# Performance work log

Hardware: AMD Instinct MI355X
Metric: run time of the kernel (lower is better)

Reference implementation:

```python
import jax, jax.numpy as jnp
import numpy as np

B, D, F, K = 16384, 768, 8192, 32

def setup_inputs() -> dict:
    key = jax.random.key(0)
    k0, k1, k2 = jax.random.split(key, 3)
    x = jax.random.normal(k0, (B, D), dtype=jnp.float32)
    # encoder weight ~ orthogonal-ish scale; exact init scheme doesn't affect the math being tested
    W_enc = jax.random.normal(k1, (F, D), dtype=jnp.float32) / np.sqrt(D)
    b_enc = jnp.zeros((F,), dtype=jnp.float32)
    W_dec = jax.random.normal(k2, (D, F), dtype=jnp.float32)
    # torch init normalizes decoder.weight rows (dim=1)
    W_dec = W_dec / jnp.linalg.norm(W_dec, axis=1, keepdims=True)
    dec_bias = jnp.zeros((D,), dtype=jnp.float32)
    return {"x": x, "W_enc": W_enc, "b_enc": b_enc, "W_dec": W_dec, "dec_bias": dec_bias, "k": K}


def reference(x, W_enc, b_enc, W_dec, dec_bias, k):
    # encode: center, linear, relu
    x_centered = x - dec_bias                              # [B, D]
    acts = jax.nn.relu(jnp.einsum('bd,fd->bf', x_centered, W_enc) + b_enc)  # [B, F]
    # topk + scatter into dense sparse code
    vals, idx = jax.lax.top_k(acts, k)                     # [B, k]
    rows = jnp.arange(acts.shape[0])[:, None]              # [B, 1]
    sparse_code = jnp.zeros_like(acts).at[rows, idx].set(vals)  # [B, F]
    # decode: dense GEMM over mostly-zero code + bias
    reconstruction = jnp.einsum('bf,df->bd', sparse_code, W_dec) + dec_bias  # [B, D]
    return reconstruction, sparse_code
```

## Files before the change

kernel.cpp:

```cpp
#include <hip/hip_runtime.h>

#define NB 16384
#define ND 768
#define NF 8192
#define CMAX 512
#define AMAX 128
#define MARG 0.07f

typedef __attribute__((ext_vector_type(8))) short bf16x8;
typedef __attribute__((ext_vector_type(4))) float f32x4;
typedef __attribute__((ext_vector_type(4))) unsigned int u32x4;
typedef __attribute__((ext_vector_type(2))) float f32x2;

__device__ inline unsigned short f2bf(float f) {
  unsigned u = __float_as_uint(f);
  unsigned r = (u + 0x7FFFu + ((u >> 16) & 1u)) >> 16;
  return (unsigned short)r;
}
__device__ inline float bfbits2f(unsigned u16) { return __uint_as_float(u16 << 16); }

__global__ __launch_bounds__(256) void cvt_bf16_k(const float* __restrict__ in,
                                                  unsigned short* __restrict__ out) {
  size_t t = (size_t)blockIdx.x * 256 + threadIdx.x;
  const float4* i4 = (const float4*)in;
  float4 a = i4[t * 2], b = i4[t * 2 + 1];
  ushort4 lo = make_ushort4(f2bf(a.x), f2bf(a.y), f2bf(a.z), f2bf(a.w));
  ushort4 hi = make_ushort4(f2bf(b.x), f2bf(b.y), f2bf(b.z), f2bf(b.w));
  ((ushort4*)out)[t * 2] = lo;
  ((ushort4*)out)[t * 2 + 1] = hi;
}

__global__ __launch_bounds__(256) void beta_k(const float* __restrict__ W_enc,
                                              const float* __restrict__ b_enc,
                                              const float* __restrict__ dec_bias,
                                              float* __restrict__ beta) {
  int f = blockIdx.x * 4 + (threadIdx.x >> 6);
  int lane = threadIdx.x & 63;
  const float* wr = W_enc + (size_t)f * ND;
  float s = 0.f;
  for (int d = lane; d < ND; d += 64) s += dec_bias[d] * wr[d];
  for (int off = 32; off; off >>= 1) s += __shfl_down(s, off);
  if (lane == 0) beta[f] = b_enc[f] - s;
}

__global__ __launch_bounds__(256) void transpose_bf_k(const float* __restrict__ in,
                                                      unsigned short* __restrict__ out) {
  __shared__ float tile[32][33];
  int lx = threadIdx.x & 31;
  int ty = threadIdx.x >> 5;
  int x = blockIdx.x * 32 + lx;
  for (int j = ty; j < 32; j += 8) {
    int y = blockIdx.y * 32 + j;
    tile[j][lx] = in[(size_t)y * NF + x];
  }
  __syncthreads();
  int xo = blockIdx.y * 32 + lx;
  for (int j = ty; j < 32; j += 8) {
    int yo = blockIdx.x * 32 + j;
    out[(size_t)yo * ND + xo] = f2bf(tile[lx][j]);
  }
}

__global__ __launch_bounds__(256) void enc_gemm_bf16(
    const unsigned short* __restrict__ Xb, const unsigned short* __restrict__ Wb,
    const float* __restrict__ beta, unsigned short* __restrict__ acts,
    unsigned short* __restrict__ tmax) {
  __shared__ __align__(1024) unsigned short SL[2][128 * 64];
  unsigned short* As = SL[0];
  unsigned short* Bs = SL[1];
  const int tid = threadIdx.x;
  const int wave = tid >> 6, lane = tid & 63;
  const int wm = wave >> 1, wn = wave & 1;

  const int orig = blockIdx.y * gridDim.x + blockIdx.x;
  const int xcd = orig & 7;
  const int local = orig >> 3;
  const int tcol = local >> 4;
  const int trow = (xcd << 4) + (local & 15);
  const int brow = trow << 7;
  const int bcol = tcol << 7;

  f32x4 acc[4][4] = {};

  const int srow = tid >> 3;
  const int scol = (((tid & 7) ^ ((tid >> 3) & 7)) << 3);
  const unsigned short* gA = Xb + (size_t)(brow + srow) * ND + scol;
  const unsigned short* gB = Wb + (size_t)(bcol + srow) * ND + scol;

  for (int kt = 0; kt < ND; kt += 64) {
#pragma unroll
    for (int i = 0; i < 4; ++i) {
      __builtin_amdgcn_global_load_lds(
          (const __attribute__((address_space(1))) void*)(gA + (size_t)(i * 32) * ND + kt),
          (__attribute__((address_space(3))) void*)(As + (i * 32 + wave * 8) * 64), 16, 0, 0);
      __builtin_amdgcn_global_load_lds(
          (const __attribute__((address_space(1))) void*)(gB + (size_t)(i * 32) * ND + kt),
          (__attribute__((address_space(3))) void*)(Bs + (i * 32 + wave * 8) * 64), 16, 0, 0);
    }
    __syncthreads();
#pragma unroll
    for (int kk = 0; kk < 64; kk += 32) {
      const int chunk = (kk + ((lane >> 4) << 3)) >> 3;
      const int rA = (wm << 6) + (lane & 15);
      const int rB = (wn << 6) + (lane & 15);
      const int sw = chunk ^ (lane & 7);
      bf16x8 a[4], bvv[4];
#pragma unroll
      for (int m = 0; m < 4; ++m)
        a[m] = *(const bf16x8*)&As[(rA + (m << 4)) * 64 + (sw << 3)];
#pragma unroll
      for (int n = 0; n < 4; ++n)
        bvv[n] = *(const bf16x8*)&Bs[(rB + (n << 4)) * 64 + (sw << 3)];
#pragma unroll
      for (int m = 0; m < 4; ++m)
#pragma unroll
        for (int n = 0; n < 4; ++n)
          acc[m][n] = __builtin_amdgcn_mfma_f32_16x16x32_bf16(a[m], bvv[n], acc[m][n], 0, 0, 0);
    }
    __syncthreads();
  }

  unsigned short* S = (unsigned short*)SL;
#pragma unroll
  for (int n = 0; n < 4; ++n) {
    float bet = beta[bcol + (wn << 6) + (n << 4) + (lane & 15)];
#pragma unroll
    for (int m = 0; m < 4; ++m) {
#pragma unroll
      for (int r = 0; r < 4; ++r) {
        int row_l = (wm << 6) + (m << 4) + ((lane >> 4) << 2) + r;
        int col_l = (wn << 6) + (n << 4) + (lane & 15);
        float v = fmaxf(acc[m][n][r] + bet, 0.f);
        int slot = (col_l >> 3) ^ (row_l & 7);
        S[row_l * 128 + (slot << 3) + (col_l & 7)] = f2bf(v);
      }
    }
  }
  __syncthreads();
#pragma unroll
  for (int i = 0; i < 8; ++i) {
    int row_l = (tid >> 4) + (i << 4);
    int slot = tid & 15;
    u32x4 d = *(const u32x4*)&S[row_l * 128 + (slot << 3)];
    unsigned mx = 0;
#pragma unroll
    for (int q = 0; q < 4; ++q) {
      unsigned lo = d[q] & 0xFFFFu, hi = d[q] >> 16;
      if (lo > mx) mx = lo;
      if (hi > mx) mx = hi;
    }
#pragma unroll
    for (int off = 1; off < 16; off <<= 1) {
      unsigned o = __shfl_xor(mx, off);
      if (o > mx) mx = o;
    }
    int chunk = slot ^ (row_l & 7);
    __builtin_nontemporal_store(
        d, (u32x4*)&acts[(size_t)(brow + row_l) * NF + bcol + (chunk << 3)]);
    if (slot == 0) tmax[(size_t)(brow + row_l) * 64 + tcol] = (unsigned short)mx;
  }
}

__global__ __launch_bounds__(256) void tkth_k(const unsigned short* __restrict__ tmax,
                                              const int* __restrict__ kptr,
                                              float* __restrict__ Lthr) {
  const int wave = threadIdx.x >> 6, lane = threadIdx.x & 63;
  const int b = blockIdx.x * 4 + wave;
  int k = *kptr; k = k < 1 ? 1 : (k > 64 ? 64 : k);
  unsigned key = tmax[(size_t)b * 64 + lane];
  unsigned T = 0;
  for (int bit = 14; bit >= 0; --bit) {
    unsigned probe = T | (1u << bit);
    int c = __popcll(__ballot(key >= probe));
    if (c >= k) T = probe;
  }
  if (lane == 0) Lthr[b] = bfbits2f(T) - MARG;
}

__global__ __launch_bounds__(256, 6) void ksel_k(
    const unsigned short* __restrict__ acts, const unsigned short* __restrict__ tmax,
    const float* __restrict__ Lthr, const float* __restrict__ x,
    const float* __restrict__ W_enc, const float* __restrict__ beta,
    const unsigned short* __restrict__ WdecBf, const float* __restrict__ dec_bias,
    const int* __restrict__ kptr,
    float* __restrict__ out_rec, float* __restrict__ g_vals, int* __restrict__ g_idxs) {
  const int tid = threadIdx.x, wave = tid >> 6, lane = tid & 63;
  const int b = blockIdx.x * 4 + wave;
  int k = *kptr; k = k < 1 ? 1 : (k > 64 ? 64 : k);
  const unsigned kk = (unsigned)k;

  __shared__ int stile_s[4][64];
  __shared__ unsigned clist_s[4][CMAX];
  __shared__ unsigned long long aval_s[4][AMAX];
  __shared__ float selv_s[4][64];
  __shared__ int seli_s[4][64];
  __shared__ int ctrC_s[4], ctrW_s[4], ctrA_s[4];

  int* stile = stile_s[wave];
  unsigned* clist = clist_s[wave];
  unsigned long long* aval = aval_s[wave];
  float* selv = selv_s[wave];
  int* seli = seli_s[wave];

  if (lane == 0) { ctrC_s[wave] = 0; ctrW_s[wave] = 0; ctrA_s[wave] = 0; }
  const float Lf = Lthr[b];

  {
    unsigned short tm = tmax[(size_t)b * 64 + lane];
    bool sel = bfbits2f(tm) >= Lf;
    unsigned long long mask = __ballot(sel);
    int pos = __popcll(mask & ((1ull << lane) - 1ull));
    if (sel) stile[pos] = lane;
  }
  __syncthreads();
  const int nsel = __popcll(__ballot(bfbits2f(tmax[(size_t)b * 64 + lane]) >= Lf));

  const u32x4* row16 = (const u32x4*)(acts + (size_t)b * NF);
  for (int t = 0; t < nsel; t += 4) {
    int tt = t + (lane >> 4);
    if (tt < nsel) {
      int tile = stile[tt];
      u32x4 v = __builtin_nontemporal_load(&row16[tile * 16 + (lane & 15)]);
      int base = tile * 128 + (lane & 15) * 8;
#pragma unroll
      for (int q = 0; q < 4; ++q) {
#pragma unroll
        for (int h = 0; h < 2; ++h) {
          unsigned u = h ? (v[q] >> 16) : (v[q] & 0xFFFFu);
          if (bfbits2f(u) >= Lf) {
            int p = atomicAdd(&ctrC_s[wave], 1);
            if (p < CMAX) clist[p] = (u << 16) | (unsigned)(base + q * 2 + h);
          }
        }
      }
    }
  }
  __syncthreads();
  int n = ctrC_s[wave]; if (n > CMAX) n = CMAX;

  unsigned ks[8];
#pragma unroll
  for (int ii = 0; ii < 8; ++ii) {
    int j = lane + (ii << 6);
    ks[ii] = (j < n) ? (clist[j] >> 16) : 0u;
  }
  unsigned T = 0;
  for (int bit = 14; bit >= 0; --bit) {
    unsigned probe = T | (1u << bit);
    int c = 0;
#pragma unroll
    for (int ii = 0; ii < 8; ++ii) c += (ks[ii] >= probe);
#pragma unroll
    for (int off = 32; off; off >>= 1) c += __shfl_xor(c, off);
    if (c >= (int)kk) T = probe;
  }
  const float tauf = bfbits2f(T);
  const float thrW = tauf + MARG;
  const float thrA = tauf - MARG;

  for (int j = lane; j < n; j += 64) {
    unsigned e = clist[j];
    float v = bfbits2f(e >> 16);
    int idx = (int)(e & 0xFFFFu);
    if (v > thrW) {
      int p = atomicAdd(&ctrW_s[wave], 1);
      if (p < 63) { selv[p] = v; seli[p] = idx; }
    } else if (v >= thrA) {
      int p = atomicAdd(&ctrA_s[wave], 1);
      if (p < AMAX) aval[p] = (unsigned long long)(unsigned)idx;
    }
  }
  __syncthreads();
  int c = ctrW_s[wave]; if (c > 63) c = 63; if (c > k - 1) c = k - 1;
  int na = ctrA_s[wave]; if (na > AMAX) na = AMAX;

  float xr[12];
#pragma unroll
  for (int cc = 0; cc < 12; ++cc)
    xr[cc] = __builtin_nontemporal_load(&x[(size_t)b * ND + lane + 64 * cc]);
  for (int j = 0; j < na; j += 2) {
    int f0 = (int)(unsigned)aval[j];
    int f1 = (j + 1 < na) ? (int)(unsigned)aval[j + 1] : f0;
    const float* w0 = W_enc + (size_t)f0 * ND;
    const float* w1 = W_enc + (size_t)f1 * ND;
    float s0 = 0.f, s1 = 0.f;
#pragma unroll
    for (int cc = 0; cc < 12; ++cc) {
      s0 = fmaf(xr[cc], w0[lane + 64 * cc], s0);
      s1 = fmaf(xr[cc], w1[lane + 64 * cc], s1);
    }
#pragma unroll
    for (int off = 32; off; off >>= 1) {
      s0 += __shfl_xor(s0, off);
      s1 += __shfl_xor(s1, off);
    }
    if (lane == 0) {
      float v0 = fmaxf(s0 + beta[f0], 0.f);
      aval[j] = (((unsigned long long)__float_as_uint(v0)) << 13) | (unsigned)(8191 - f0);
      if (j + 1 < na) {
        float v1 = fmaxf(s1 + beta[f1], 0.f);
        aval[j + 1] = (((unsigned long long)__float_as_uint(v1)) << 13) | (unsigned)(8191 - f1);
      }
    }
  }
  __syncthreads();

  {
    unsigned long long p0 = (lane < na) ? aval[lane] : 0ull;
    unsigned long long p1 = (lane + 64 < na) ? aval[lane + 64] : 0ull;
    int rounds = k - c; if (rounds < 0) rounds = 0;
    for (int r = 0; r < rounds; ++r) {
      unsigned long long m = p0 > p1 ? p0 : p1;
#pragma unroll
      for (int off = 32; off; off >>= 1) {
        unsigned long long o = __shfl_xor(m, off);
        if (o > m) m = o;
      }
      if (lane == 0) {
        if (m) { selv[c + r] = __uint_as_float((unsigned)(m >> 13)); seli[c + r] = 8191 - (int)(m & 0x1FFFull); }
        else   { selv[c + r] = 0.f; seli[c + r] = 0; }
      }
      if (p0 == m) p0 = 0;
      if (p1 == m) p1 = 0;
    }
  }
  __syncthreads();

  if (lane < k) {
    g_vals[(size_t)b * 64 + lane] = selv[lane];
    g_idxs[(size_t)b * 64 + lane] = seli[lane];
  }

  float acc[12];
#pragma unroll
  for (int cc = 0; cc < 6; ++cc) {
    float2 db = *(const float2*)&dec_bias[cc * 128 + lane * 2];
    acc[2 * cc] = db.x; acc[2 * cc + 1] = db.y;
  }
#define RECON_TERM(r)                                                          \
  {                                                                            \
    int f = seli[r]; float v = selv[r];                                        \
    const unsigned short* wd = WdecBf + (size_t)f * ND;                        \
    _Pragma("unroll")                                                          \
    for (int cc = 0; cc < 6; ++cc) {                                           \
      unsigned pr = *(const unsigned*)&wd[cc * 128 + lane * 2];                \
      acc[2 * cc] = fmaf(v, bfbits2f(pr & 0xFFFFu), acc[2 * cc]);              \
      acc[2 * cc + 1] = fmaf(v, bfbits2f(pr >> 16), acc[2 * cc + 1]);          \
    }                                                                          \
  }
  if (k == 32) {
#pragma unroll
    for (int r = 0; r < 32; ++r) RECON_TERM(r)
  } else {
    for (int r = 0; r < k; ++r) RECON_TERM(r)
  }
#pragma unroll
  for (int cc = 0; cc < 6; ++cc) {
    f32x2 st = {acc[2 * cc], acc[2 * cc + 1]};
    __builtin_nontemporal_store(st, (f32x2*)&out_rec[(size_t)b * ND + cc * 128 + lane * 2]);
  }
}

__global__ __launch_bounds__(256) void d2_sparse_k(
    const float* __restrict__ g_vals, const int* __restrict__ g_idxs,
    const int* __restrict__ kptr, float* __restrict__ out_sc) {
  const int b = blockIdx.x, tid = threadIdx.x;
  int k = *kptr; k = k < 1 ? 1 : (k > 64 ? 64 : k);
  __shared__ float row[NF];
  __shared__ float sv[64];
  __shared__ int si[64];
  if (tid < k) { sv[tid] = g_vals[(size_t)b * 64 + tid]; si[tid] = g_idxs[(size_t)b * 64 + tid]; }
  float4* r4 = (float4*)row;
#pragma unroll
  for (int i = 0; i < 8; ++i) r4[tid + 256 * i] = make_float4(0.f, 0.f, 0.f, 0.f);
  __syncthreads();
  if (tid < k) row[si[tid]] = sv[tid];
  __syncthreads();
  f32x4* o4 = (f32x4*)(out_sc + (size_t)b * NF);
  const f32x4* r4v = (const f32x4*)row;
#pragma unroll
  for (int i = 0; i < 8; ++i)
    __builtin_nontemporal_store(r4v[tid + 256 * i], &o4[tid + 256 * i]);
}

extern "C" void kernel_launch(void* const* d_in, const int* in_sizes, int n_in,
                              void* d_out, int out_size, void* d_ws, size_t ws_size,
                              hipStream_t stream) {
  const float* x        = (const float*)d_in[0];
  const float* W_enc    = (const float*)d_in[1];
  const float* b_enc    = (const float*)d_in[2];
  const float* W_dec    = (const float*)d_in[3];
  const float* dec_bias = (const float*)d_in[4];
  const int*   kptr     = (const int*)d_in[5];

  float* out_rec = (float*)d_out;
  float* out_sc  = (float*)d_out + (size_t)NB * ND;

  char* scb = (char*)out_sc;
  unsigned short* acts = (unsigned short*)scb;
  unsigned short* Xbf  = (unsigned short*)(scb + 268435456);
  unsigned short* Wbf  = (unsigned short*)(scb + 293601280);

  char* ws = (char*)d_ws;
  unsigned short* WdecBf = (unsigned short*)ws;
  float* beta   = (float*)(ws + 12582912);
  float* g_vals = (float*)(ws + 12615680);
  int*   g_idxs = (int*)(ws + 16809984);
  unsigned short* tmax = (unsigned short*)(ws + 21004288);
  float* Lthr  = (float*)(ws + 23101440);

  cvt_bf16_k<<<(NB * ND) / 2048, 256, 0, stream>>>(x, Xbf);
  cvt_bf16_k<<<(NF * ND) / 2048, 256, 0, stream>>>(W_enc, Wbf);
  beta_k<<<NF / 4, 256, 0, stream>>>(W_enc, b_enc, dec_bias, beta);
  transpose_bf_k<<<dim3(NF / 32, ND / 32), 256, 0, stream>>>(W_dec, WdecBf);
  enc_gemm_bf16<<<dim3(NF / 128, NB / 128), 256, 0, stream>>>(Xbf, Wbf, beta, acts, tmax);
  tkth_k<<<NB / 4, 256, 0, stream>>>(tmax, kptr, Lthr);
  ksel_k<<<NB / 4, 256, 0, stream>>>(acts, tmax, Lthr, x, W_enc, beta, WdecBf, dec_bias,
                                     kptr, out_rec, g_vals, g_idxs);
  d2_sparse_k<<<NB, 256, 0, stream>>>(g_vals, g_idxs, kptr, out_sc);
}
```

Baseline: 601.9 us.

## Collect above-threshold candidates in GEMM epilogue, skip per-row acts rescan

The encoder GEMM epilogue now appends every activation at or above a fixed threshold (2.0) to a per-row global candidate list using global atomics. The top-k selection kernel reads this list directly instead of recomputing a tile threshold and rescanning the bf16 activation rows, and the separate threshold kernel is removed. A fallback path runs the old scan for any block where the list overflowed, held too few entries, or the resulting tau is too close to the fixed threshold. The cost is many global atomics in the GEMM epilogue, an extra zeroing kernel, and a threshold constant tuned to the input distribution.

```diff
diff --git a/kernel.cpp b/kernel.cpp
--- a/kernel.cpp
+++ b/kernel.cpp
@@ -6,6 +6,8 @@
 #define CMAX 512
 #define AMAX 128
 #define MARG 0.07f
+#define THETA0 2.0f
+#define THETA0_BITS 0x4000u
 
 typedef __attribute__((ext_vector_type(8))) short bf16x8;
 typedef __attribute__((ext_vector_type(4))) float f32x4;
@@ -18,6 +20,10 @@
   return (unsigned short)r;
 }
 __device__ inline float bfbits2f(unsigned u16) { return __uint_as_float(u16 << 16); }
+
+__global__ __launch_bounds__(256) void zerocnt_k(unsigned* __restrict__ gcnt) {
+  gcnt[blockIdx.x * 256 + threadIdx.x] = 0u;
+}
 
 __global__ __launch_bounds__(256) void cvt_bf16_k(const float* __restrict__ in,
                                                   unsigned short* __restrict__ out) {
@@ -64,7 +70,8 @@
 __global__ __launch_bounds__(256) void enc_gemm_bf16(
     const unsigned short* __restrict__ Xb, const unsigned short* __restrict__ Wb,
     const float* __restrict__ beta, unsigned short* __restrict__ acts,
-    unsigned short* __restrict__ tmax) {
+    unsigned short* __restrict__ tmax,
+    unsigned* __restrict__ gcnt, unsigned* __restrict__ glist) {
   __shared__ __align__(1024) unsigned short SL[2][128 * 64];
   unsigned short* As = SL[0];
   unsigned short* Bs = SL[1];
@@ -131,8 +138,15 @@
         int row_l = (wm << 6) + (m << 4) + ((lane >> 4) << 2) + r;
         int col_l = (wn << 6) + (n << 4) + (lane & 15);
         float v = fmaxf(acc[m][n][r] + bet, 0.f);
+        unsigned short ub = f2bf(v);
         int slot = (col_l >> 3) ^ (row_l & 7);
-        S[row_l * 128 + (slot << 3) + (col_l & 7)] = f2bf(v);
+        S[row_l * 128 + (slot << 3) + (col_l & 7)] = ub;
+        if (ub >= (unsigned short)THETA0_BITS) {
+          unsigned p = atomicAdd(&gcnt[brow + row_l], 1u);
+          if (p < CMAX)
+            glist[(size_t)(brow + row_l) * CMAX + p] =
+                ((unsigned)ub << 16) | (unsigned)(bcol + col_l);
+        }
       }
     }
   }
@@ -161,28 +175,12 @@
   }
 }
 
-__global__ __launch_bounds__(256) void tkth_k(const unsigned short* __restrict__ tmax,
-                                              const int* __restrict__ kptr,
-                                              float* __restrict__ Lthr) {
-  const int wave = threadIdx.x >> 6, lane = threadIdx.x & 63;
-  const int b = blockIdx.x * 4 + wave;
-  int k = *kptr; k = k < 1 ? 1 : (k > 64 ? 64 : k);
-  unsigned key = tmax[(size_t)b * 64 + lane];
-  unsigned T = 0;
-  for (int bit = 14; bit >= 0; --bit) {
-    unsigned probe = T | (1u << bit);
-    int c = __popcll(__ballot(key >= probe));
-    if (c >= k) T = probe;
-  }
-  if (lane == 0) Lthr[b] = bfbits2f(T) - MARG;
-}
-
 __global__ __launch_bounds__(256, 6) void ksel_k(
     const unsigned short* __restrict__ acts, const unsigned short* __restrict__ tmax,
-    const float* __restrict__ Lthr, const float* __restrict__ x,
-    const float* __restrict__ W_enc, const float* __restrict__ beta,
-    const unsigned short* __restrict__ WdecBf, const float* __restrict__ dec_bias,
-    const int* __restrict__ kptr,
+    const unsigned* __restrict__ gcnt, const unsigned* __restrict__ glist,
+    const float* __restrict__ x, const float* __restrict__ W_enc,
+    const float* __restrict__ beta, const unsigned short* __restrict__ WdecBf,
+    const float* __restrict__ dec_bias, const int* __restrict__ kptr,
     float* __restrict__ out_rec, float* __restrict__ g_vals, int* __restrict__ g_idxs) {
   const int tid = threadIdx.x, wave = tid >> 6, lane = tid & 63;
   const int b = blockIdx.x * 4 + wave;
@@ -195,6 +193,7 @@
   __shared__ float selv_s[4][64];
   __shared__ int seli_s[4][64];
   __shared__ int ctrC_s[4], ctrW_s[4], ctrA_s[4];
+  __shared__ int blkFb;
 
   int* stile = stile_s[wave];
   unsigned* clist = clist_s[wave];
@@ -202,41 +201,13 @@
   float* selv = selv_s[wave];
   int* seli = seli_s[wave];
 
+  if (tid == 0) blkFb = 0;
   if (lane == 0) { ctrC_s[wave] = 0; ctrW_s[wave] = 0; ctrA_s[wave] = 0; }
-  const float Lf = Lthr[b];
-
-  {
-    unsigned short tm = tmax[(size_t)b * 64 + lane];
-    bool sel = bfbits2f(tm) >= Lf;
-    unsigned long long mask = __ballot(sel);
-    int pos = __popcll(mask & ((1ull << lane) - 1ull));
-    if (sel) stile[pos] = lane;
-  }
-  __syncthreads();
-  const int nsel = __popcll(__ballot(bfbits2f(tmax[(size_t)b * 64 + lane]) >= Lf));
-
-  const u32x4* row16 = (const u32x4*)(acts + (size_t)b * NF);
-  for (int t = 0; t < nsel; t += 4) {
-    int tt = t + (lane >> 4);
-    if (tt < nsel) {
-      int tile = stile[tt];
-      u32x4 v = __builtin_nontemporal_load(&row16[tile * 16 + (lane & 15)]);
-      int base = tile * 128 + (lane & 15) * 8;
-#pragma unroll
-      for (int q = 0; q < 4; ++q) {
-#pragma unroll
-        for (int h = 0; h < 2; ++h) {
-          unsigned u = h ? (v[q] >> 16) : (v[q] & 0xFFFFu);
-          if (bfbits2f(u) >= Lf) {
-            int p = atomicAdd(&ctrC_s[wave], 1);
-            if (p < CMAX) clist[p] = (u << 16) | (unsigned)(base + q * 2 + h);
-          }
-        }
-      }
-    }
-  }
-  __syncthreads();
-  int n = ctrC_s[wave]; if (n > CMAX) n = CMAX;
+
+  const int raw = (int)gcnt[b];
+  int n = raw < CMAX ? raw : CMAX;
+  for (int j = lane; j < n; j += 64) clist[j] = glist[(size_t)b * CMAX + j];
+  __syncthreads();
 
   unsigned ks[8];
 #pragma unroll
@@ -254,7 +225,70 @@
     for (int off = 32; off; off >>= 1) c += __shfl_xor(c, off);
     if (c >= (int)kk) T = probe;
   }
-  const float tauf = bfbits2f(T);
+  float tauf = bfbits2f(T);
+
+  bool valid = (raw <= CMAX) && (n >= k) && (tauf >= THETA0 + MARG);
+  if (lane == 0 && !valid) atomicOr(&blkFb, 1);
+  __syncthreads();
+
+  if (blkFb) {
+    unsigned tm = tmax[(size_t)b * 64 + lane];
+    unsigned T2 = 0;
+    for (int bit = 14; bit >= 0; --bit) {
+      unsigned probe = T2 | (1u << bit);
+      int c = __popcll(__ballot(tm >= probe));
+      if (c >= k) T2 = probe;
+    }
+    const float Lf = bfbits2f(T2) - MARG;
+    if (lane == 0) ctrC_s[wave] = 0;
+    {
+      bool sel = bfbits2f(tm) >= Lf;
+      unsigned long long mask = __ballot(sel);
+      int pos = __popcll(mask & ((1ull << lane) - 1ull));
+      if (sel) stile[pos] = lane;
+    }
+    __syncthreads();
+    const int nsel = __popcll(__ballot(bfbits2f(tm) >= Lf));
+    const u32x4* row16 = (const u32x4*)(acts + (size_t)b * NF);
+    for (int t = 0; t < nsel; t += 4) {
+      int tt = t + (lane >> 4);
+      if (tt < nsel) {
+        int tile = stile[tt];
+        u32x4 v = __builtin_nontemporal_load(&row16[tile * 16 + (lane & 15)]);
+        int base = tile * 128 + (lane & 15) * 8;
+#pragma unroll
+        for (int q = 0; q < 4; ++q) {
+#pragma unroll
+          for (int h = 0; h < 2; ++h) {
+            unsigned u = h ? (v[q] >> 16) : (v[q] & 0xFFFFu);
+            if (bfbits2f(u) >= Lf) {
+              int p = atomicAdd(&ctrC_s[wave], 1);
+              if (p < CMAX) clist[p] = (u << 16) | (unsigned)(base + q * 2 + h);
+            }
+          }
+        }
+      }
+    }
+    __syncthreads();
+    n = ctrC_s[wave]; if (n > CMAX) n = CMAX;
+#pragma unroll
+    for (int ii = 0; ii < 8; ++ii) {
+      int j = lane + (ii << 6);
+      ks[ii] = (j < n) ? (clist[j] >> 16) : 0u;
+    }
+    T = 0;
+    for (int bit = 14; bit >= 0; --bit) {
+      unsigned probe = T | (1u << bit);
+      int c = 0;
+#pragma unroll
+      for (int ii = 0; ii < 8; ++ii) c += (ks[ii] >= probe);
+#pragma unroll
+      for (int off = 32; off; off >>= 1) c += __shfl_xor(c, off);
+      if (c >= (int)kk) T = probe;
+    }
+    tauf = bfbits2f(T);
+  }
+
   const float thrW = tauf + MARG;
   const float thrA = tauf - MARG;
 
@@ -397,9 +431,11 @@
   float* out_sc  = (float*)d_out + (size_t)NB * ND;
 
   char* scb = (char*)out_sc;
-  unsigned short* acts = (unsigned short*)scb;
-  unsigned short* Xbf  = (unsigned short*)(scb + 268435456);
-  unsigned short* Wbf  = (unsigned short*)(scb + 293601280);
+  unsigned short* acts  = (unsigned short*)scb;
+  unsigned short* Xbf   = (unsigned short*)(scb + 268435456);
+  unsigned short* Wbf   = (unsigned short*)(scb + 293601280);
+  unsigned*       glist = (unsigned*)(scb + 306184192);
+  unsigned*       gcnt  = (unsigned*)(scb + 339738624);
 
   char* ws = (char*)d_ws;
   unsigned short* WdecBf = (unsigned short*)ws;
@@ -407,15 +443,15 @@
   float* g_vals = (float*)(ws + 12615680);
   int*   g_idxs = (int*)(ws + 16809984);
   unsigned short* tmax = (unsigned short*)(ws + 21004288);
-  float* Lthr  = (float*)(ws + 23101440);
-
+
+  zerocnt_k<<<64, 256, 0, stream>>>(gcnt);
   cvt_bf16_k<<<(NB * ND) / 2048, 256, 0, stream>>>(x, Xbf);
   cvt_bf16_k<<<(NF * ND) / 2048, 256, 0, stream>>>(W_enc, Wbf);
   beta_k<<<NF / 4, 256, 0, stream>>>(W_enc, b_enc, dec_bias, beta);
   transpose_bf_k<<<dim3(NF / 32, ND / 32), 256, 0, stream>>>(W_dec, WdecBf);
-  enc_gemm_bf16<<<dim3(NF / 128, NB / 128), 256, 0, stream>>>(Xbf, Wbf, beta, acts, tmax);
-  tkth_k<<<NB / 4, 256, 0, stream>>>(tmax, kptr, Lthr);
-  ksel_k<<<NB / 4, 256, 0, stream>>>(acts, tmax, Lthr, x, W_enc, beta, WdecBf, dec_bias,
-                                     kptr, out_rec, g_vals, g_idxs);
+  enc_gemm_bf16<<<dim3(NF / 128, NB / 128), 256, 0, stream>>>(Xbf, Wbf, beta, acts,
+                                                              tmax, gcnt, glist);
+  ksel_k<<<NB / 4, 256, 0, stream>>>(acts, tmax, gcnt, glist, x, W_enc, beta, WdecBf,
+                                     dec_bias, kptr, out_rec, g_vals, g_idxs);
   d2_sparse_k<<<NB, 256, 0, stream>>>(g_vals, g_idxs, kptr, out_sc);
 }
```

Measured after the change: 940.8 us. +56.3%, slower.

## Emit fixed-threshold candidate lists from encoder GEMM instead of full bf16 activations

Applied to the files above, without the earlier changes.

The encoder GEMM no longer writes the full bf16 activation matrix and per-tile maxima. In its epilogue it keeps only activations above a fixed threshold of 2.0, appending up to 16 per row-tile into a compact candidate list. The threshold kernel is removed and the selection kernel reads these compact lists directly. The GEMM main loop also gains double-buffered LDS staging. When a row's candidates are insufficient or overflow, a slow block-wide fallback recomputes the full row in fp32. This relies on the fixed threshold suiting the data distribution and adds a costly path for rows where it does not.

```diff
diff --git a/kernel.cpp b/kernel.cpp
--- a/kernel.cpp
+++ b/kernel.cpp
@@ -4,8 +4,12 @@
 #define ND 768
 #define NF 8192
 #define CMAX 512
+#define SEGW 16
+#define GSEG 1024
 #define AMAX 128
 #define MARG 0.07f
+#define THETA0 2.0f
+#define THETA0_BITS 0x4000u
 
 typedef __attribute__((ext_vector_type(8))) short bf16x8;
 typedef __attribute__((ext_vector_type(4))) float f32x4;
@@ -63,11 +67,11 @@
 
 __global__ __launch_bounds__(256) void enc_gemm_bf16(
     const unsigned short* __restrict__ Xb, const unsigned short* __restrict__ Wb,
-    const float* __restrict__ beta, unsigned short* __restrict__ acts,
-    unsigned short* __restrict__ tmax) {
-  __shared__ __align__(1024) unsigned short SL[2][128 * 64];
-  unsigned short* As = SL[0];
-  unsigned short* Bs = SL[1];
+    const float* __restrict__ beta, unsigned* __restrict__ glist) {
+  __shared__ __align__(1024) unsigned short As[2][128 * 64];
+  __shared__ __align__(1024) unsigned short Bs[2][128 * 64];
+  __shared__ unsigned wseg[128][SEGW];
+  __shared__ unsigned wcnt[128];
   const int tid = threadIdx.x;
   const int wave = tid >> 6, lane = tid & 63;
   const int wm = wave >> 1, wn = wave & 1;
@@ -87,17 +91,27 @@
   const unsigned short* gA = Xb + (size_t)(brow + srow) * ND + scol;
   const unsigned short* gB = Wb + (size_t)(bcol + srow) * ND + scol;
 
-  for (int kt = 0; kt < ND; kt += 64) {
-#pragma unroll
-    for (int i = 0; i < 4; ++i) {
-      __builtin_amdgcn_global_load_lds(
-          (const __attribute__((address_space(1))) void*)(gA + (size_t)(i * 32) * ND + kt),
-          (__attribute__((address_space(3))) void*)(As + (i * 32 + wave * 8) * 64), 16, 0, 0);
-      __builtin_amdgcn_global_load_lds(
-          (const __attribute__((address_space(1))) void*)(gB + (size_t)(i * 32) * ND + kt),
-          (__attribute__((address_space(3))) void*)(Bs + (i * 32 + wave * 8) * 64), 16, 0, 0);
-    }
-    __syncthreads();
+#pragma unroll
+  for (int i = 0; i < 8; ++i) ((unsigned*)wseg)[tid + 256 * i] = 0u;
+  if (tid < 128) wcnt[tid] = 0u;
+
+#define STAGE(bufsel, kt)                                                      \
+  _Pragma("unroll")                                                            \
+  for (int i = 0; i < 4; ++i) {                                                \
+    __builtin_amdgcn_global_load_lds(                                          \
+        (const __attribute__((address_space(1))) void*)(gA + (size_t)(i * 32) * ND + (kt)), \
+        (__attribute__((address_space(3))) void*)(As[bufsel] + (i * 32 + wave * 8) * 64), 16, 0, 0); \
+    __builtin_amdgcn_global_load_lds(                                          \
+        (const __attribute__((address_space(1))) void*)(gB + (size_t)(i * 32) * ND + (kt)), \
+        (__attribute__((address_space(3))) void*)(Bs[bufsel] + (i * 32 + wave * 8) * 64), 16, 0, 0); \
+  }
+
+  STAGE(0, 0)
+  __syncthreads();
+  int cur = 0;
+#pragma unroll 1
+  for (int step = 0; step < 12; ++step) {
+    if (step < 11) { STAGE(cur ^ 1, (step + 1) * 64) }
 #pragma unroll
     for (int kk = 0; kk < 64; kk += 32) {
       const int chunk = (kk + ((lane >> 4) << 3)) >> 3;
@@ -107,20 +121,22 @@
       bf16x8 a[4], bvv[4];
 #pragma unroll
       for (int m = 0; m < 4; ++m)
-        a[m] = *(const bf16x8*)&As[(rA + (m << 4)) * 64 + (sw << 3)];
+        a[m] = *(const bf16x8*)&As[cur][(rA + (m << 4)) * 64 + (sw << 3)];
 #pragma unroll
       for (int n = 0; n < 4; ++n)
-        bvv[n] = *(const bf16x8*)&Bs[(rB + (n << 4)) * 64 + (sw << 3)];
+        bvv[n] = *(const bf16x8*)&Bs[cur][(rB + (n << 4)) * 64 + (sw << 3)];
 #pragma unroll
       for (int m = 0; m < 4; ++m)
 #pragma unroll
         for (int n = 0; n < 4; ++n)
           acc[m][n] = __builtin_amdgcn_mfma_f32_16x16x32_bf16(a[m], bvv[n], acc[m][n], 0, 0, 0);
     }
-    __syncthreads();
-  }
-
-  unsigned short* S = (unsigned short*)SL;
+    if (step < 11) {
+      __syncthreads();
+      cur ^= 1;
+    }
+  }
+
 #pragma unroll
   for (int n = 0; n < 4; ++n) {
     float bet = beta[bcol + (wn << 6) + (n << 4) + (lane & 15)];
@@ -131,111 +147,79 @@
         int row_l = (wm << 6) + (m << 4) + ((lane >> 4) << 2) + r;
         int col_l = (wn << 6) + (n << 4) + (lane & 15);
         float v = fmaxf(acc[m][n][r] + bet, 0.f);
-        int slot = (col_l >> 3) ^ (row_l & 7);
-        S[row_l * 128 + (slot << 3) + (col_l & 7)] = f2bf(v);
-      }
-    }
-  }
-  __syncthreads();
-#pragma unroll
-  for (int i = 0; i < 8; ++i) {
-    int row_l = (tid >> 4) + (i << 4);
-    int slot = tid & 15;
-    u32x4 d = *(const u32x4*)&S[row_l * 128 + (slot << 3)];
-    unsigned mx = 0;
-#pragma unroll
-    for (int q = 0; q < 4; ++q) {
-      unsigned lo = d[q] & 0xFFFFu, hi = d[q] >> 16;
-      if (lo > mx) mx = lo;
-      if (hi > mx) mx = hi;
-    }
-#pragma unroll
-    for (int off = 1; off < 16; off <<= 1) {
-      unsigned o = __shfl_xor(mx, off);
-      if (o > mx) mx = o;
-    }
-    int chunk = slot ^ (row_l & 7);
-    __builtin_nontemporal_store(
-        d, (u32x4*)&acts[(size_t)(brow + row_l) * NF + bcol + (chunk << 3)]);
-    if (slot == 0) tmax[(size_t)(brow + row_l) * 64 + tcol] = (unsigned short)mx;
-  }
-}
-
-__global__ __launch_bounds__(256) void tkth_k(const unsigned short* __restrict__ tmax,
-                                              const int* __restrict__ kptr,
-                                              float* __restrict__ Lthr) {
-  const int wave = threadIdx.x >> 6, lane = threadIdx.x & 63;
-  const int b = blockIdx.x * 4 + wave;
-  int k = *kptr; k = k < 1 ? 1 : (k > 64 ? 64 : k);
-  unsigned key = tmax[(size_t)b * 64 + lane];
-  unsigned T = 0;
-  for (int bit = 14; bit >= 0; --bit) {
-    unsigned probe = T | (1u << bit);
-    int c = __popcll(__ballot(key >= probe));
-    if (c >= k) T = probe;
-  }
-  if (lane == 0) Lthr[b] = bfbits2f(T) - MARG;
+        unsigned short ub = f2bf(v);
+        if (ub >= (unsigned short)THETA0_BITS) {
+          unsigned p = atomicAdd(&wcnt[row_l], 1u);
+          if (p < SEGW) wseg[row_l][p] = ((unsigned)ub << 16) | (unsigned)(bcol + col_l);
+        }
+      }
+    }
+  }
+  __syncthreads();
+  {
+    int row = tid >> 1;
+    int sbase = (tid & 1) << 3;
+    u32x4 v0 = *(const u32x4*)&wseg[row][sbase];
+    u32x4 v1 = *(const u32x4*)&wseg[row][sbase + 4];
+    if (sbase == 0 && wcnt[row] > SEGW) v0[0] = 0xFFFFFFFFu;
+    unsigned* dst = &glist[(size_t)(brow + row) * GSEG + (tcol << 4)];
+    __builtin_nontemporal_store(v0, (u32x4*)&dst[sbase]);
+    __builtin_nontemporal_store(v1, (u32x4*)&dst[sbase + 4]);
+  }
 }
 
 __global__ __launch_bounds__(256, 6) void ksel_k(
-    const unsigned short* __restrict__ acts, const unsigned short* __restrict__ tmax,
-    const float* __restrict__ Lthr, const float* __restrict__ x,
-    const float* __restrict__ W_enc, const float* __restrict__ beta,
-    const unsigned short* __restrict__ WdecBf, const float* __restrict__ dec_bias,
-    const int* __restrict__ kptr,
+    const unsigned* __restrict__ glist,
+    const float* __restrict__ x, const float* __restrict__ W_enc,
+    const float* __restrict__ beta, const unsigned short* __restrict__ WdecBf,
+    const float* __restrict__ dec_bias, const int* __restrict__ kptr,
     float* __restrict__ out_rec, float* __restrict__ g_vals, int* __restrict__ g_idxs) {
   const int tid = threadIdx.x, wave = tid >> 6, lane = tid & 63;
   const int b = blockIdx.x * 4 + wave;
   int k = *kptr; k = k < 1 ? 1 : (k > 64 ? 64 : k);
   const unsigned kk = (unsigned)k;
 
-  __shared__ int stile_s[4][64];
   __shared__ unsigned clist_s[4][CMAX];
   __shared__ unsigned long long aval_s[4][AMAX];
   __shared__ float selv_s[4][64];
   __shared__ int seli_s[4][64];
   __shared__ int ctrC_s[4], ctrW_s[4], ctrA_s[4];
-
-  int* stile = stile_s[wave];
+  __shared__ int blkFb;
+  __shared__ float fb_x[ND];
+  __shared__ unsigned long long fbl[512];
+  __shared__ unsigned fb_thrmax[256];
+  __shared__ unsigned long long fb_red[4];
+  __shared__ unsigned fb_cnt4[4];
+  __shared__ unsigned fbcnt;
+
   unsigned* clist = clist_s[wave];
   unsigned long long* aval = aval_s[wave];
   float* selv = selv_s[wave];
   int* seli = seli_s[wave];
 
+  if (tid == 0) blkFb = 0;
   if (lane == 0) { ctrC_s[wave] = 0; ctrW_s[wave] = 0; ctrA_s[wave] = 0; }
-  const float Lf = Lthr[b];
-
+
+  bool bad = false;
   {
-    unsigned short tm = tmax[(size_t)b * 64 + lane];
-    bool sel = bfbits2f(tm) >= Lf;
-    unsigned long long mask = __ballot(sel);
-    int pos = __popcll(mask & ((1ull << lane) - 1ull));
-    if (sel) stile[pos] = lane;
-  }
-  __syncthreads();
-  const int nsel = __popcll(__ballot(bfbits2f(tmax[(size_t)b * 64 + lane]) >= Lf));
-
-  const u32x4* row16 = (const u32x4*)(acts + (size_t)b * NF);
-  for (int t = 0; t < nsel; t += 4) {
-    int tt = t + (lane >> 4);
-    if (tt < nsel) {
-      int tile = stile[tt];
-      u32x4 v = __builtin_nontemporal_load(&row16[tile * 16 + (lane & 15)]);
-      int base = tile * 128 + (lane & 15) * 8;
+    const u32x4* seg4 = (const u32x4*)(glist + (size_t)b * GSEG);
+#pragma unroll
+    for (int ii = 0; ii < 4; ++ii) {
+      u32x4 e4 = __builtin_nontemporal_load(&seg4[lane + (ii << 6)]);
 #pragma unroll
       for (int q = 0; q < 4; ++q) {
-#pragma unroll
-        for (int h = 0; h < 2; ++h) {
-          unsigned u = h ? (v[q] >> 16) : (v[q] & 0xFFFFu);
-          if (bfbits2f(u) >= Lf) {
+        unsigned e = e4[q];
+        if (e) {
+          if ((e & 0xFFFFu) >= (unsigned)NF) bad = true;
+          else {
             int p = atomicAdd(&ctrC_s[wave], 1);
-            if (p < CMAX) clist[p] = (u << 16) | (unsigned)(base + q * 2 + h);
+            if (p < CMAX) clist[p] = e;
           }
         }
       }
     }
   }
-  __syncthreads();
+  bad = (__ballot(bad) != 0ull);
   int n = ctrC_s[wave]; if (n > CMAX) n = CMAX;
 
   unsigned ks[8];
@@ -254,58 +238,62 @@
     for (int off = 32; off; off >>= 1) c += __shfl_xor(c, off);
     if (c >= (int)kk) T = probe;
   }
-  const float tauf = bfbits2f(T);
-  const float thrW = tauf + MARG;
-  const float thrA = tauf - MARG;
-
-  for (int j = lane; j < n; j += 64) {
-    unsigned e = clist[j];
-    float v = bfbits2f(e >> 16);
-    int idx = (int)(e & 0xFFFFu);
-    if (v > thrW) {
-      int p = atomicAdd(&ctrW_s[wave], 1);
-      if (p < 63) { selv[p] = v; seli[p] = idx; }
-    } else if (v >= thrA) {
-      int p = atomicAdd(&ctrA_s[wave], 1);
-      if (p < AMAX) aval[p] = (unsigned long long)(unsigned)idx;
-    }
-  }
-  __syncthreads();
-  int c = ctrW_s[wave]; if (c > 63) c = 63; if (c > k - 1) c = k - 1;
-  int na = ctrA_s[wave]; if (na > AMAX) na = AMAX;
-
-  float xr[12];
-#pragma unroll
-  for (int cc = 0; cc < 12; ++cc)
-    xr[cc] = __builtin_nontemporal_load(&x[(size_t)b * ND + lane + 64 * cc]);
-  for (int j = 0; j < na; j += 2) {
-    int f0 = (int)(unsigned)aval[j];
-    int f1 = (j + 1 < na) ? (int)(unsigned)aval[j + 1] : f0;
-    const float* w0 = W_enc + (size_t)f0 * ND;
-    const float* w1 = W_enc + (size_t)f1 * ND;
-    float s0 = 0.f, s1 = 0.f;
-#pragma unroll
-    for (int cc = 0; cc < 12; ++cc) {
-      s0 = fmaf(xr[cc], w0[lane + 64 * cc], s0);
-      s1 = fmaf(xr[cc], w1[lane + 64 * cc], s1);
-    }
-#pragma unroll
-    for (int off = 32; off; off >>= 1) {
-      s0 += __shfl_xor(s0, off);
-      s1 += __shfl_xor(s1, off);
-    }
-    if (lane == 0) {
-      float v0 = fmaxf(s0 + beta[f0], 0.f);
-      aval[j] = (((unsigned long long)__float_as_uint(v0)) << 13) | (unsigned)(8191 - f0);
-      if (j + 1 < na) {
-        float v1 = fmaxf(s1 + beta[f1], 0.f);
-        aval[j + 1] = (((unsigned long long)__float_as_uint(v1)) << 13) | (unsigned)(8191 - f1);
-      }
-    }
-  }
-  __syncthreads();
-
-  {
+  float tauf = bfbits2f(T);
+
+  bool valid = !bad && (n >= k) && (tauf >= THETA0 + MARG);
+  if (lane == 0 && !valid) atomicOr(&blkFb, 1);
+  __syncthreads();
+
+  if (!blkFb) {
+    const float thrW = tauf + MARG;
+    const float thrA = tauf - MARG;
+    for (int j = lane; j < n; j += 64) {
+      unsigned e = clist[j];
+      float v = bfbits2f(e >> 16);
+      int idx = (int)(e & 0xFFFFu);
+      if (v > thrW) {
+        int p = atomicAdd(&ctrW_s[wave], 1);
+        if (p < 63) { selv[p] = v; seli[p] = idx; }
+      } else if (v >= thrA) {
+        int p = atomicAdd(&ctrA_s[wave], 1);
+        if (p < AMAX) aval[p] = (unsigned long long)(unsigned)idx;
+      }
+    }
+    __syncthreads();
+    int c = ctrW_s[wave]; if (c > 63) c = 63; if (c > k - 1) c = k - 1;
+    int na = ctrA_s[wave]; if (na > AMAX) na = AMAX;
+
+    float xr[12];
+#pragma unroll
+    for (int cc = 0; cc < 12; ++cc)
+      xr[cc] = __builtin_nontemporal_load(&x[(size_t)b * ND + lane + 64 * cc]);
+    for (int j = 0; j < na; j += 2) {
+      int f0 = (int)(unsigned)aval[j];
+      int f1 = (j + 1 < na) ? (int)(unsigned)aval[j + 1] : f0;
+      const float* w0 = W_enc + (size_t)f0 * ND;
+      const float* w1 = W_enc + (size_t)f1 * ND;
+      float s0 = 0.f, s1 = 0.f;
+#pragma unroll
+      for (int cc = 0; cc < 12; ++cc) {
+        s0 = fmaf(xr[cc], w0[lane + 64 * cc], s0);
+        s1 = fmaf(xr[cc], w1[lane + 64 * cc], s1);
+      }
+#pragma unroll
+      for (int off = 32; off; off >>= 1) {
+        s0 += __shfl_xor(s0, off);
+        s1 += __shfl_xor(s1, off);
+      }
+      if (lane == 0) {
+        float v0 = fmaxf(s0 + beta[f0], 0.f);
+        aval[j] = (((unsigned long long)__float_as_uint(v0)) << 13) | (unsigned)(8191 - f0);
+        if (j + 1 < na) {
+          float v1 = fmaxf(s1 + beta[f1], 0.f);
+          aval[j + 1] = (((unsigned long long)__float_as_uint(v1)) << 13) | (unsigned)(8191 - f1);
+        }
+      }
+    }
+    __syncthreads();
+
     unsigned long long p0 = (lane < na) ? aval[lane] : 0ull;
     unsigned long long p1 = (lane + 64 < na) ? aval[lane + 64] : 0ull;
     int rounds = k - c; if (rounds < 0) rounds = 0;
@@ -323,8 +311,78 @@
       if (p0 == m) p0 = 0;
       if (p1 == m) p1 = 0;
     }
-  }
-  __syncthreads();
+    __syncthreads();
+  } else {
+    for (int r = 0; r < 4; ++r) {
+      const int row = blockIdx.x * 4 + r;
+      fb_x[tid] = x[(size_t)row * ND + tid];
+      fb_x[tid + 256] = x[(size_t)row * ND + tid + 256];
+      fb_x[tid + 512] = x[(size_t)row * ND + tid + 512];
+      __syncthreads();
+      unsigned mymax = 0u;
+      for (int j = 0; j < 32; ++j) {
+        int f = tid * 32 + j;
+        const float* w = W_enc + (size_t)f * ND;
+        float s = 0.f;
+#pragma unroll 8
+        for (int d = 0; d < ND; ++d) s = fmaf(fb_x[d], w[d], s);
+        unsigned bits = __float_as_uint(fmaxf(s + beta[f], 0.f));
+        if (bits > mymax) mymax = bits;
+      }
+      fb_thrmax[tid] = mymax;
+      __syncthreads();
+      unsigned L = 0;
+      for (int bit = 30; bit >= 0; --bit) {
+        unsigned probe = L | (1u << bit);
+        unsigned long long bl = __ballot(fb_thrmax[tid] >= probe);
+        if (lane == 0) fb_cnt4[wave] = (unsigned)__popcll(bl);
+        __syncthreads();
+        unsigned tot = fb_cnt4[0] + fb_cnt4[1] + fb_cnt4[2] + fb_cnt4[3];
+        if (tot >= kk) L = probe;
+        __syncthreads();
+      }
+      if (tid == 0) fbcnt = 0u;
+      __syncthreads();
+      for (int j = 0; j < 32; ++j) {
+        int f = tid * 32 + j;
+        const float* w = W_enc + (size_t)f * ND;
+        float s = 0.f;
+#pragma unroll 8
+        for (int d = 0; d < ND; ++d) s = fmaf(fb_x[d], w[d], s);
+        unsigned bits = __float_as_uint(fmaxf(s + beta[f], 0.f));
+        if (bits >= L) {
+          unsigned p = atomicAdd(&fbcnt, 1u);
+          if (p < 512) fbl[p] = (((unsigned long long)bits) << 13) | (unsigned)(8191 - f);
+        }
+      }
+      __syncthreads();
+      int n2 = (int)(fbcnt < 512u ? fbcnt : 512u);
+      for (int rr = 0; rr < k; ++rr) {
+        unsigned long long best = 0ull;
+        for (int j2 = tid; j2 < n2; j2 += 256)
+          if (fbl[j2] > best) best = fbl[j2];
+#pragma unroll
+        for (int off = 32; off; off >>= 1) {
+          unsigned long long o = __shfl_xor(best, off);
+          if (o > best) best = o;
+        }
+        if (lane == 0) fb_red[wave] = best;
+        __syncthreads();
+        unsigned long long m = fb_red[0];
+#pragma unroll
+        for (int w2 = 1; w2 < 4; ++w2)
+          if (fb_red[w2] > m) m = fb_red[w2];
+        if (tid == 0) {
+          if (m) { selv_s[r][rr] = __uint_as_float((unsigned)(m >> 13)); seli_s[r][rr] = 8191 - (int)(m & 0x1FFFull); }
+          else   { selv_s[r][rr] = 0.f; seli_s[r][rr] = 0; }
+        }
+        for (int j2 = tid; j2 < n2; j2 += 256)
+          if (fbl[j2] == m) fbl[j2] = 0ull;
+        __syncthreads();
+      }
+      __syncthreads();
+    }
+  }
 
   if (lane < k) {
     g_vals[(size_t)b * 64 + lane] = selv[lane];
@@ -397,25 +455,22 @@
   float* out_sc  = (float*)d_out + (size_t)NB * ND;
 
   char* scb = (char*)out_sc;
-  unsigned short* acts = (unsigned short*)scb;
-  unsigned short* Xbf  = (unsigned short*)(scb + 268435456);
-  unsigned short* Wbf  = (unsigned short*)(scb + 293601280);
+  unsigned*       glist = (unsigned*)scb;
+  unsigned short* Xbf   = (unsigned short*)(scb + 67108864);
+  unsigned short* Wbf   = (unsigned short*)(scb + 92274688);
 
   char* ws = (char*)d_ws;
   unsigned short* WdecBf = (unsigned short*)ws;
   float* beta   = (float*)(ws + 12582912);
   float* g_vals = (float*)(ws + 12615680);
   int*   g_idxs = (int*)(ws + 16809984);
-  unsigned short* tmax = (unsigned short*)(ws + 21004288);
-  float* Lthr  = (float*)(ws + 23101440);
 
   cvt_bf16_k<<<(NB * ND) / 2048, 256, 0, stream>>>(x, Xbf);
   cvt_bf16_k<<<(NF * ND) / 2048, 256, 0, stream>>>(W_enc, Wbf);
   beta_k<<<NF / 4, 256, 0, stream>>>(W_enc, b_enc, dec_bias, beta);
   transpose_bf_k<<<dim3(NF / 32, ND / 32), 256, 0, stream>>>(W_dec, WdecBf);
-  enc_gemm_bf16<<<dim3(NF / 128, NB / 128), 256, 0, stream>>>(Xbf, Wbf, beta, acts, tmax);
-  tkth_k<<<NB / 4, 256, 0, stream>>>(tmax, kptr, Lthr);
-  ksel_k<<<NB / 4, 256, 0, stream>>>(acts, tmax, Lthr, x, W_enc, beta, WdecBf, dec_bias,
-                                     kptr, out_rec, g_vals, g_idxs);
+  enc_gemm_bf16<<<dim3(NF / 128, NB / 128), 256, 0, stream>>>(Xbf, Wbf, beta, glist);
+  ksel_k<<<NB / 4, 256, 0, stream>>>(glist, x, W_enc, beta, WdecBf, dec_bias, kptr,
+                                     out_rec, g_vals, g_idxs);
   d2_sparse_k<<<NB, 256, 0, stream>>>(g_vals, g_idxs, kptr, out_sc);
 }
```

After: 646.9 us. 1.07x slower.
